# Kernel tuning notes

Measured on AMD Instinct MI355X. Metric: run time of the kernel, lower is better.

Reference implementation:

```python
import jax, jax.numpy as jnp
import numpy as np
from math import factorial

# ---- static sizes from S2ConvNet_original ----
B_IN, B1, B2 = 30, 10, 6   # bandwidths: input S2 grid, after conv1 (SO3), after conv2 (SO3)
F1, F2, FOUT = 20, 40, 10
BATCH = 128


def _wigner_d(l, beta):
    """Wigner small-d matrix d^l_{m',m}(beta); rows m'=-l..l, cols m=-l..l."""
    cb, sb = np.cos(beta / 2.0), np.sin(beta / 2.0)
    d = np.zeros((2 * l + 1, 2 * l + 1))
    for i, mp in enumerate(range(-l, l + 1)):
        for j, m in enumerate(range(-l, l + 1)):
            pref = np.sqrt(float(factorial(l + mp) * factorial(l - mp) * factorial(l + m) * factorial(l - m)))
            acc = 0.0
            for s in range(max(0, m - mp), min(l + m, l - mp) + 1):
                den = factorial(l + m - s) * factorial(s) * factorial(mp - m + s) * factorial(l - mp - s)
                acc += ((-1.0) ** (mp - m + s) / den) * cb ** (2 * l + m - mp - 2 * s) * sb ** (mp - m + 2 * s)
            d[i, j] = pref * acc
    return d


def _dh_quad(b):
    """Driscoll-Healy beta grid / weights: sum_j w_j g(beta_j) ~ int_0^pi g(b) sin(b) db."""
    j = np.arange(2 * b)
    beta = np.pi * (2 * j + 1) / (4 * b)
    k = np.arange(b)[:, None]
    w = (2.0 / b) * np.sin(beta) * np.sum(np.sin((2 * k + 1) * beta[None, :]) / (2 * k + 1), axis=0)
    return beta, w


def _s2_grid(max_beta=np.pi / 8, n_alpha=8, n_beta=3):
    beta = np.arange(1, n_beta + 1) * max_beta / n_beta
    alpha = np.linspace(0, 2 * np.pi, n_alpha, endpoint=False)
    Bm, Am = np.meshgrid(beta, alpha, indexing='ij')
    return np.stack([Bm.ravel(), Am.ravel()], 1)  # [24, 2]


def _so3_grid(max_beta=np.pi / 8, max_gamma=2 * np.pi, n_alpha=8, n_beta=3, n_gamma=8):
    beta = np.arange(1, n_beta + 1) * max_beta / n_beta
    alpha = np.linspace(0, 2 * np.pi, n_alpha, endpoint=False)
    pre_gamma = np.linspace(0, max_gamma, n_gamma, endpoint=False)
    Bm, Am, Cm = np.meshgrid(beta, alpha, pre_gamma, indexing='ij')
    return np.stack([Bm.ravel(), Am.ravel(), (Cm - Am).ravel()], 1)  # [192, 3]


# ---------- conv1: S2 analysis (b 30 -> 10) ----------
_beta30, _qw30 = _dh_quad(B_IN)
_A1 = np.concatenate(
    [np.stack([_wigner_d(l, bb)[:, l] for bb in _beta30])  # d^l_{m,0}(beta_j): [60, 2l+1]
     * (_qw30 * (2 * np.pi / (2 * B_IN)))[:, None]
     for l in range(B1)], axis=1)  # [60, 100]
_A1J = jnp.asarray(_A1.astype(np.float32))
_M1 = np.concatenate([np.arange(-l, l + 1) for l in range(B1)])
_M1_IDX = np.mod(_M1, 2 * B_IN)

_g1 = _s2_grid()
_Y1 = np.concatenate(
    [np.stack([_wigner_d(l, bb)[:, l] for bb in _g1[:, 0]])
     * np.exp(-1j * np.outer(_g1[:, 1], np.arange(-l, l + 1)))
     for l in range(B1)], axis=1)  # [24, 100] complex
_Y1J = jnp.asarray(_Y1.astype(np.complex64))
_SC1 = float(1.0 / np.sqrt(len(_g1) * 1 * (B1 ** 4) / (B_IN ** 2)))

# ---------- SO3 synthesis tables at b=10 ----------
_beta10, _qw10 = _dh_quad(B1)
_D1S = [jnp.asarray(((2 * l + 1) * np.stack([_wigner_d(l, bb) for bb in _beta10])).astype(np.float32)) for l in range(B1)]
_FM1 = [np.mod(np.arange(-l, l + 1), 2 * B1) for l in range(B1)]

# ---------- conv2: SO3 analysis (b 10 -> 6) ----------
_W3 = np.concatenate(
    [(np.stack([_wigner_d(l, bb) for bb in _beta10])  # [20, 2l+1, 2l+1]
      * (_qw10 * (2 * np.pi / (2 * B1)) ** 2)[:, None, None]).reshape(2 * B1, -1)
     for l in range(B2)], axis=1)  # [20, 286]
_W3J = jnp.asarray(_W3.astype(np.float32))
_M2 = np.concatenate([np.repeat(np.arange(-l, l + 1), 2 * l + 1) for l in range(B2)])
_N2 = np.concatenate([np.tile(np.arange(-l, l + 1), 2 * l + 1) for l in range(B2)])
_M2_IDX = np.mod(_M2, 2 * B1)
_N2_IDX = np.mod(_N2, 2 * B1)

_g2 = _so3_grid()
_Y2 = np.concatenate(
    [np.stack([_wigner_d(l, bb) for bb in _g2[:, 0]]).reshape(len(_g2), -1)
     * (np.exp(-1j * np.outer(_g2[:, 1], np.arange(-l, l + 1)))[:, :, None]
        * np.exp(-1j * np.outer(_g2[:, 2], np.arange(-l, l + 1)))[:, None, :]).reshape(len(_g2), -1)
     for l in range(B2)], axis=1)  # [192, 286] complex: D^l_{mn}(alpha,beta,gamma)
_Y2J = jnp.asarray(_Y2.astype(np.complex64))
_SC2 = float(1.0 / np.sqrt(len(_g2) * F1 * (B2 ** 3) / (B1 ** 3)))

# ---------- SO3 synthesis tables at b=6 + integration weights ----------
_beta6, _qw6 = _dh_quad(B2)
_D2S = [jnp.asarray(((2 * l + 1) * np.stack([_wigner_d(l, bb) for bb in _beta6])).astype(np.float32)) for l in range(B2)]
_FM2 = [np.mod(np.arange(-l, l + 1), 2 * B2) for l in range(B2)]
_W_INT = jnp.asarray((_qw6 * (2 * np.pi / (2 * B2)) ** 2).astype(np.float32))


def _forward(x, k1, bias1, k2, bias2, w_out, b_lin):
    Bn = x.shape[0]
    # ===== conv1: S2 correlation -> function on SO(3) at b=10 =====
    xf = jnp.fft.fft(x.astype(jnp.complex64), axis=-1)                 # FFT over alpha: [B,1,60,60]
    xhat = jnp.einsum('bfjs,js->sbf', xf[..., _M1_IDX], _A1J)          # [100,B,1] S2 spectrum
    k1h = jnp.einsum('iop,ps->sio', (k1 * _SC1).astype(jnp.complex64), _Y1J)  # [100,1,F1]
    Ffreq = jnp.zeros((Bn, F1, 2 * B1, 2 * B1, 2 * B1), jnp.complex64)  # [B,F1,beta,m,n]
    for l in range(B1):
        s0, s1 = l * l, (l + 1) * (l + 1)
        # z^l_{mn} = sum_fin xhat^l_m conj(khat^l_n)  (outer product per degree l)
        zl = jnp.einsum('mbi,nio->bmno', xhat[s0:s1], jnp.conj(k1h[s0:s1]))
        fb = jnp.einsum('bmno,jmn->bojmn', zl, _D1S[l])                # (2l+1) d^l_{mn}(beta_j)
        Ffreq = Ffreq.at[:, :, :, _FM1[l][:, None], _FM1[l][None, :]].add(fb)
    x1 = jnp.fft.ifft2(Ffreq, axes=(-2, -1)).real * float((2 * B1) ** 2)  # synth over alpha,gamma
    x1 = jax.nn.relu(x1 + bias1[None, :, None, None, None])            # [B,F1,20,20,20]
    # ===== conv2: SO(3) correlation -> b=6 =====
    x1f = jnp.fft.fft2(x1.astype(jnp.complex64), axes=(-2, -1))        # FFT over alpha,gamma
    xhat2 = jnp.einsum('bfjs,js->sbf', x1f[:, :, :, _M2_IDX, _N2_IDX], _W3J)  # [286,B,F1]
    k2h = jnp.einsum('iop,ps->sio', (k2 * _SC2).astype(jnp.complex64), _Y2J)  # [286,F1,F2]
    Ffreq2 = jnp.zeros((Bn, F2, 2 * B2, 2 * B2, 2 * B2), jnp.complex64)
    base = 0
    for l in range(B2):
        L = 2 * l + 1
        xl = xhat2[base:base + L * L].reshape(L, L, Bn, F1)            # [m,k,B,Fin]
        gl = jnp.conj(k2h[base:base + L * L].reshape(L, L, F1, F2))    # [n,k,Fin,Fout]
        zl = jnp.einsum('mkbi,nkio->bmno', xl, gl)                     # z^l = xhat^l ghat^l^H
        fb = jnp.einsum('bmno,jmn->bojmn', zl, _D2S[l])
        Ffreq2 = Ffreq2.at[:, :, :, _FM2[l][:, None], _FM2[l][None, :]].add(fb)
        base += L * L
    x2 = jnp.fft.ifft2(Ffreq2, axes=(-2, -1)).real * float((2 * B2) ** 2)
    x2 = jax.nn.relu(x2 + bias2[None, :, None, None, None])            # [B,F2,12,12,12]
    # ===== so3_integrate + linear head =====
    feat = jnp.einsum('bfjkp,j->bf', x2, _W_INT)                       # [B,F2]
    return feat @ w_out.T + b_lin


def setup_inputs() -> dict:
    key = jax.random.key(0)
    ks = jax.random.split(key, 4)
    return {
        'x': jax.random.normal(ks[0], (BATCH, 1, 2 * B_IN, 2 * B_IN), jnp.float32),
        'k1': jax.random.normal(ks[1], (1, F1, len(_g1)), jnp.float32),
        'bias1': jnp.zeros((F1,), jnp.float32),
        'k2': jax.random.normal(ks[2], (F1, F2, len(_g2)), jnp.float32),
        'bias2': jnp.zeros((F2,), jnp.float32),
        'w_out': jax.random.normal(ks[3], (FOUT, F2), jnp.float32) / np.sqrt(F2).astype(np.float32),
        'b_lin': jnp.zeros((FOUT,), jnp.float32),
    }


def reference(x, k1, bias1, k2, bias2, w_out, b_lin):
    return _forward(x, k1, bias1, k2, bias2, w_out, b_lin)
```

## Files before the change

kernel.cpp:

```cpp
#include <hip/hip_runtime.h>
#include <math.h>

#define PI_D 3.14159265358979323846

#define BATCH 128
#define F1 20
#define F2 40
#define FOUT 10
#define NS1 100
#define NS2 286
#define NH2 146

typedef float v2f __attribute__((ext_vector_type(2)));
#define PKFMA(a,b,c) __builtin_elementwise_fma((a),(b),(c))
#define SW(v) __builtin_shufflevector((v),(v),1,0)
static __device__ __forceinline__ v2f bc2(float s){ return (v2f){s,s}; }
static __device__ __forceinline__ v2f ldv(const float2* p){ return *(const v2f*)p; }

#define GLOAD_LDS16(g,l) __builtin_amdgcn_global_load_lds( \
  (const __attribute__((address_space(1))) void*)(g), \
  (__attribute__((address_space(3))) void*)(l), 16, 0, 0)

__constant__ int ZB10c[11] = {0,1,10,35,84,165,286,455,680,969,1330};
__constant__ int B2OFFc[7] = {0,1,10,35,84,165,286};
__constant__ int HOFFc[7]  = {0,1,6,19,44,85,146};
__constant__ float2 E8c[8] = {
  { 1.f, 0.f}, { 0.70710678118654752f,-0.70710678118654752f},
  { 0.f,-1.f}, {-0.70710678118654752f,-0.70710678118654752f},
  {-1.f, 0.f}, {-0.70710678118654752f, 0.70710678118654752f},
  { 0.f, 1.f}, { 0.70710678118654752f, 0.70710678118654752f}};

#define WFENCE do{ __builtin_amdgcn_sched_barrier(0); \
  asm volatile("s_waitcnt lgkmcnt(0)" ::: "memory"); \
  __builtin_amdgcn_sched_barrier(0); }while(0)

__device__ inline void h_decode(int h, int& l, int& m, int& n){
  l=0; while(HOFFc[l+1]<=h) ++l;
  int r=h-HOFFc[l], L=2*l+1;
  if(r<l+1){ n=0; m=r; }
  else { int q=r-(l+1); n=q/L+1; m=q%L-l; }
}

__device__ inline double ipow_d(double x, int n){ double r=1.0; for(int i=0;i<n;++i) r*=x; return r; }
__device__ inline double dfact(int n){ double r=1.0; for(int i=2;i<=n;++i) r*=(double)i; return r; }

__device__ double wigd(int l, int mp, int m, double beta){
  double cb=cos(0.5*beta), sb=sin(0.5*beta);
  double pref=sqrt(dfact(l+mp)*dfact(l-mp)*dfact(l+m)*dfact(l-m));
  int s0 = (m-mp>0) ? (m-mp) : 0;
  int s1 = (l+m < l-mp) ? (l+m) : (l-mp);
  double acc=0.0;
  for(int s=s0;s<=s1;++s){
    double den=dfact(l+m-s)*dfact(s)*dfact(mp-m+s)*dfact(l-mp-s);
    double t=ipow_d(cb,2*l+m-mp-2*s)*ipow_d(sb,mp-m+2*s)/den;
    acc += ((mp-m+s)&1)? -t : t;
  }
  return pref*acc;
}

__device__ double dhw(int b, int j){
  double beta=PI_D*(2*j+1)/(4.0*b);
  double s=0.0;
  for(int k=0;k<b;++k) s += sin((2*k+1)*beta)/(2*k+1);
  return (2.0/b)*sin(beta)*s;
}

__device__ inline float2 cmulc(float2 a, float2 b){
  return make_float2(a.x*b.x + a.y*b.y, a.y*b.x - a.x*b.y);
}

__global__ void gen_all(float* A1, float* D1SJ, float* W3H, float* D2SJ,
                        float* D3_2, float* D3_1, float* WINT,
                        float2* E60, float2* E20, float2* E12,
                        unsigned* zLUT, unsigned* xh2LUT, unsigned* h2LUT,
                        unsigned short* fhLUT, unsigned* aLUT){
  __shared__ double dhwS[60];
  int blk=blockIdx.x, t=threadIdx.x;
  if(blk<24){
    if(t<60) dhwS[t]=dhw(30,t);
    __syncthreads();
    int idx=blk*256+t;
    if(idx<6000){
      int j=idx/NS1, s=idx%NS1;
      int l=0; while((l+1)*(l+1)<=s) ++l;
      int m=s-l*l-l;
      double beta=PI_D*(2*j+1)/120.0;
      A1[idx]=(float)(wigd(l,m,0,beta)*dhwS[j]*(2.0*PI_D/60.0));
    }
  } else if(blk<76){
    int idx=(blk-24)*256+t; if(idx>=13300) return;
    int j=idx/1330, s=idx%1330;
    int l=0; while(ZB10c[l+1]<=s) ++l;
    int r=s-ZB10c[l]; int L=2*l+1;
    int mi=r/L, ni=r%L;
    double beta=PI_D*(2*j+1)/40.0;
    float v=(float)((2*l+1)*wigd(l,mi-l,ni-l,beta));
    D1SJ[j*1330+s]=v;
    int s2=ZB10c[l]+(2*l-mi)*L+ni;
    D1SJ[(19-j)*1330+s2]=(ni&1)? -v : v;
  } else if(blk<82){
    if(t<20) dhwS[t]=dhw(10,t);
    __syncthreads();
    int idx=(blk-76)*256+t;
    if(idx<10*NH2){
      int j=idx/NH2, h=idx%NH2;
      int l,m,n; h_decode(h,l,m,n);
      double beta=PI_D*(2*j+1)/40.0;
      double c=2.0*PI_D/20.0;
      float v=(float)(wigd(l,m,n,beta)*dhwS[j]*c*c);
      W3H[j*NH2+h]=v;
      if(n==0){
        W3H[(19-j)*NH2+h]=((l+m)&1)? -v : v;
      } else {
        int L=2*l+1;
        int hp=HOFFc[l]+(l+1)+(n-1)*L+(l-m);
        W3H[(19-j)*NH2+hp]=((l+n)&1)? -v : v;
      }
    }
  } else if(blk<89){
    int idx=(blk-82)*256+t; if(idx>=1716) return;
    int j=idx/286, s=idx%286;
    int l=0; while(B2OFFc[l+1]<=s) ++l;
    int r=s-B2OFFc[l]; int L=2*l+1;
    int mi=r/L, ni=r%L;
    double beta=PI_D*(2*j+1)/24.0;
    float v=(float)((2*l+1)*wigd(l,mi-l,ni-l,beta));
    D2SJ[j*286+s]=v;
    int s2=B2OFFc[l]+(2*l-mi)*L+ni;
    D2SJ[(11-j)*286+s2]=(ni&1)? -v : v;
  } else if(blk<93){
    int idx=(blk-89)*256+t; if(idx>=3*286) return;
    int bi=idx/286, s=idx%286;
    int l=0; while(B2OFFc[l+1]<=s) ++l;
    int r=s-B2OFFc[l]; int L=2*l+1;
    int mi=r/L, ni=r%L;
    double beta=(bi+1)*(PI_D/8.0)/3.0;
    D3_2[idx]=(float)wigd(l,mi-l,ni-l,beta);
  } else if(blk<95){
    int idx=(blk-93)*256+t; if(idx>=3*100) return;
    int bi=idx/100, s=idx%100;
    int l=0; while((l+1)*(l+1)<=s) ++l;
    int m=s-l*l-l;
    double beta=(bi+1)*(PI_D/8.0)/3.0;
    D3_1[idx]=(float)wigd(l,m,0,beta);
  } else if(blk==95){
    if(t<12){ double c=2.0*PI_D/12.0; WINT[t]=(float)(dhw(6,t)*c*c); }
    if(t<60){ double a=2.0*PI_D*t/60.0; E60[t]=make_float2((float)cos(a),(float)sin(a)); }
    if(t<20){ double a=2.0*PI_D*t/20.0; E20[t]=make_float2((float)cos(a),(float)sin(a)); }
    if(t<12){ double a=2.0*PI_D*t/12.0; E12[t]=make_float2((float)cos(a),(float)sin(a)); }
  } else if(blk<102){
    int idx=(blk-96)*256+t; if(idx>=1330) return;
    int l=0; while(ZB10c[l+1]<=idx) ++l;
    int r=idx-ZB10c[l], L=2*l+1;
    int mi=r/L, ni=r%L;
    unsigned s1x=(unsigned)(l*l+mi), s1k=(unsigned)(l*l+ni);
    zLUT[idx]=s1x|(s1k<<16);
  } else if(blk==102){
    if(t<146){
      int l,m,n; h_decode(t,l,m,n);
      int L=2*l+1;
      int s2 =B2OFFc[l]+(m+l)*L+(n+l);
      int s2p=B2OFFc[l]+(l-m)*L+(l-n);
      unsigned sg=(unsigned)((m+n)&1);
      xh2LUT[t]=(unsigned)s2 | ((unsigned)s2p<<10) | (sg<<20);
      h2LUT[t]=(unsigned)l | ((unsigned)(m+l)<<4) | ((unsigned)(n+l)<<8) | ((unsigned)s2<<12);
      fhLUT[t]=(unsigned short)((n==0)? m : 6+(n-1)*11+(m+5));
    }
  } else {
    if(t==0){
      int idx=0;
      for(int lm=0;lm<10;++lm){
        for(int m=0;m<10;++m){
          int nlo=(m==0)?0:-9;
          for(int n=nlo;n<10;++n){
            int an=n<0?-n:n;
            int lmin=m>an?m:an;
            if(lmin!=lm) continue;
            int L=2*lm+1;
            int zi=ZB10c[lm]+(m+lm)*L+(n+lm);
            aLUT[idx++]=(unsigned)zi | ((unsigned)m<<11) | ((unsigned)(n+9)<<15) | ((unsigned)lm<<20);
          }
        }
      }
    }
  }
}

__global__ __launch_bounds__(256) void front_k(const float* __restrict__ x,
    const float* __restrict__ k1, const float* __restrict__ k2,
    const float2* __restrict__ E60, const float* __restrict__ A1,
    const float* __restrict__ D3_1,
    float2* __restrict__ XHAT, float2* __restrict__ K1H, float2* __restrict__ KA){
  __shared__ float2 E8s[8];
  int blk=blockIdx.x, t=threadIdx.x;
  if(blk<128){
    __shared__ __align__(16) float xs[3600];
    __shared__ float2 E60s[60];
    __shared__ float2 XFs[1140];
    if(t<60){ float2 e=E60[t]; E60s[t]=make_float2(e.x,-e.y); }
    {
      const float4* src=(const float4*)(x+blk*3600);
      float4* dst=(float4*)xs;
      for(int i=t;i<900;i+=256) GLOAD_LDS16(src+i, dst+(i&~63));
    }
    __syncthreads();
    for(int idx=t; idx<1140; idx+=256){
      int j=idx/19, mi=idx%19;
      int step=(mi<9)? mi+51 : mi-9;
      bool modd = ((mi&1)==0);
      const float* xr=xs+j*60;
      v2f acc={0.f,0.f};
      int k=0;
      for(int a=0;a<30;++a){
        float xv = modd ? (xr[a]-xr[a+30]) : (xr[a]+xr[a+30]);
        acc=PKFMA(bc2(xv), ldv(&E60s[k]), acc);
        k+=step; if(k>=60)k-=60;
      }
      XFs[idx]=make_float2(acc.x,acc.y);
    }
    __syncthreads();
    for(int s=t; s<100; s+=256){
      int l=0; while((l+1)*(l+1)<=s) ++l;
      int m=s-l*l-l;
      const float2* xf=&XFs[m+9];
      v2f acc={0.f,0.f};
      for(int j=0;j<60;++j){
        acc=PKFMA(bc2(A1[j*NS1+s]), ldv(&xf[j*19]), acc);
      }
      XHAT[blk*NS1+s]=make_float2(acc.x,acc.y);
    }
  } else if(blk<136){
    if(t<8) E8s[t]=E8c[t];
    __syncthreads();
    int idx=(blk-128)*256+t;
    if(idx<F1*NS1){
      int o=idx/NS1, s=idx%NS1;
      int l=0; while((l+1)*(l+1)<=s) ++l;
      int m=s-l*l-l;
      int mm=m&7;
      v2f acc={0.f,0.f};
      for(int bi=0;bi<3;++bi){
        v2f sum={0.f,0.f};
        int q=0;
        #pragma unroll
        for(int ai=0;ai<8;++ai){
          sum=PKFMA(bc2(k1[o*24+bi*8+ai]), ldv(&E8s[q]), sum);
          q=(q+mm)&7;
        }
        acc=PKFMA(bc2(D3_1[bi*100+s]), sum, acc);
      }
      const float SC1f = 0.06123724356957945f;
      K1H[idx]=make_float2(acc.x*SC1f, acc.y*SC1f);
    }
  } else {
    if(t<8) E8s[t]=E8c[t];
    __syncthreads();
    int idx=(blk-136)*256+t;
    if(idx<153600){
      int ai=idx&7, q=(idx>>3)&7;
      int r2=idx>>6;
      int bi=r2%3, io=r2/3;
      const float* kp=k2+(size_t)io*192+bi*64+ai*8;
      v2f acc={0.f,0.f};
      int ph=0;
      #pragma unroll
      for(int gi=0;gi<8;++gi){
        acc=PKFMA(bc2(kp[gi]), ldv(&E8s[ph]), acc);
        ph=(ph+q)&7;
      }
      KA[(size_t)io*192+bi*64+q*8+ai]=make_float2(acc.x,acc.y);
    }
  }
}

__global__ __launch_bounds__(512,6) void fused1(
    const float2* __restrict__ XHAT, const float2* __restrict__ K1H,
    const float* __restrict__ D1SJ, const float* __restrict__ W3H,
    const float2* __restrict__ E20, const float* __restrict__ bias1,
    const unsigned* __restrict__ zLUT, const unsigned* __restrict__ xh2LUT,
    const unsigned short* __restrict__ fhLUT, const unsigned* __restrict__ aLUT,
    float2* __restrict__ XH2){
  const int b=blockIdx.x, o=blockIdx.y, t=threadIdx.x;
  const int ln=t&63, w=t>>6;
  __shared__ __align__(16) float2 zS[1330];
  __shared__ __align__(16) float2 TWE2[400];
  __shared__ __align__(16) float2 regA[8][200];
  __shared__ __align__(16) float2 regB[8][190];

  for(int idx=t; idx<400; idx+=512){
    int r=idx/20, c=idx%20;
    TWE2[idx]=E20[(r*c)%20];
  }
  {
    float2* st=regA[0];
    if(t<100) st[t]=XHAT[b*NS1+t];
    else if(t<200) st[t]=K1H[o*NS1+(t-100)];
  }
  __syncthreads();
  {
    const float2* st=regA[0];
    for(int idx=t; idx<1330; idx+=512){
      unsigned u=zLUT[idx];
      v2f xa=ldv(&st[u&0xffff]);
      v2f kb=ldv(&st[100+(u>>16)]);
      v2f p1=xa*kb, p2=xa*SW(kb);
      zS[idx]=make_float2(p1.x+p1.y, p2.y-p2.x);
    }
  }
  __syncthreads();

  const float bb1=bias1[o];
  float2* G  = regA[w];
  float*  vbF= (float*)regA[w];
  float2* Fq = regA[w];
  float*  RB = (float*)regB[w];
  float*  Sx = RB;
  float*  Sy = RB+180;
  float*  T0f= RB+360;
  float2* U_T= regB[w];
  v2f fa0={0.f,0.f}, fa1=fa0, fa2=fa0;

  const int BROW[19]={11,12,13,14,15,16,17,18,19,0,1,2,3,4,5,6,7,8,9};

  for(int jq=0;jq<3;++jq){
    const int j=jq*8+w;
    const bool act=(j<20);
    const float* Dg=D1SJ + (act? j*1330 : 0);
    if(act) for(int idx=ln; idx<181; idx+=64){
      unsigned au=aLUT[idx];
      int zi=au&2047;
      int m=(au>>11)&15, n9=(au>>15)&31, l=(au>>20)&15;
      int L=2*l+1;
      int m2=2*m+2;
      v2f a0={0.f,0.f};
      for(; l<10; ++l){
        a0=PKFMA(ldv(&zS[zi]), bc2(Dg[zi]), a0);
        zi += L*L + 2*L + m2; L += 2;
      }
      *(v2f*)&G[m*19+n9]=a0;
    }
    WFENCE;
    if(act){
    if(ln<45){
      int mb=ln/5+1, gp=(ln%5)*2;
      const float2* Gr=&G[mb*19];
      v2f E1a={0.f,0.f},E2a=E1a,O1a=E1a,O2a=E1a;
      v2f E1b=E1a,E2b=E1a,O1b=E1a,O2b=E1a;
      #pragma unroll
      for(int c=0;c<19;++c){
        v2f gv=ldv(&Gr[c]);
        const float* er=(const float*)&TWE2[BROW[c]*20+gp];
        float4 e01=*(const float4*)er;
        v2f e0={e01.x,e01.y}, e1={e01.z,e01.w};
        if(c&1){
          E1a=PKFMA(gv,e0,E1a); E2a=PKFMA(gv,SW(e0),E2a);
          E1b=PKFMA(gv,e1,E1b); E2b=PKFMA(gv,SW(e1),E2b);
        } else {
          O1a=PKFMA(gv,e0,O1a); O2a=PKFMA(gv,SW(e0),O2a);
          O1b=PKFMA(gv,e1,O1b); O2b=PKFMA(gv,SW(e1),O2b);
        }
      }
      int si=(mb-1)*20+gp;
      float exa=E1a.x-E1a.y, oxa=O1a.x-O1a.y;
      float eya=E2a.x+E2a.y, oya=O2a.x+O2a.y;
      float exb=E1b.x-E1b.y, oxb=O1b.x-O1b.y;
      float eyb=E2b.x+E2b.y, oyb=O2b.x+O2b.y;
      *(v2f*)&Sx[si]   =(v2f){2.f*(exa+oxa), 2.f*(exb+oxb)};
      *(v2f*)&Sx[si+10]=(v2f){2.f*(exa-oxa), 2.f*(exb-oxb)};
      *(v2f*)&Sy[si]   =(v2f){2.f*(eya+oya), 2.f*(eyb+oyb)};
      *(v2f*)&Sy[si+10]=(v2f){2.f*(eya-oya), 2.f*(eyb-oyb)};
    } else if(ln<50){
      int gt=(ln-45)*2;
      float g0x=G[9].x;
      float Ea=0.f,Eb=0.f,Oa=0.f,Ob=0.f;
      #pragma unroll
      for(int n=1;n<10;++n){
        float2 gv=G[9+n];
        const float* er=(const float*)&TWE2[n*20+gt];
        float4 e01=*(const float4*)er;
        float ra=gv.x*e01.x-gv.y*e01.y;
        float rb=gv.x*e01.z-gv.y*e01.w;
        if((n&1)==0){ Ea+=ra; Eb+=rb; } else { Oa+=ra; Ob+=rb; }
      }
      T0f[gt]   =g0x+2.f*(Ea+Oa);
      T0f[gt+1] =g0x+2.f*(Eb+Ob);
      T0f[gt+10]=g0x+2.f*(Ea-Oa);
      T0f[gt+11]=g0x+2.f*(Eb-Ob);
    }
    }
    WFENCE;
    if(act && ln<50){
      int a=ln/5, g0=(ln%5)*4;
      v2f i01={T0f[g0]+bb1, T0f[g0+1]+bb1};
      v2f i23={T0f[g0+2]+bb1, T0f[g0+3]+bb1};
      v2f P01={0.f,0.f},P23=P01,Q01=P01,Q23=P01;
      #pragma unroll
      for(int m=1;m<10;++m){
        float2 e=TWE2[a*20+m];
        v2f sx01=*(const v2f*)&Sx[(m-1)*20+g0];
        v2f sx23=*(const v2f*)&Sx[(m-1)*20+g0+2];
        v2f sy01=*(const v2f*)&Sy[(m-1)*20+g0];
        v2f sy23=*(const v2f*)&Sy[(m-1)*20+g0+2];
        if(m&1){
          Q01=PKFMA(bc2(e.x),sx01,Q01); Q01=PKFMA(bc2(-e.y),sy01,Q01);
          Q23=PKFMA(bc2(e.x),sx23,Q23); Q23=PKFMA(bc2(-e.y),sy23,Q23);
        } else {
          P01=PKFMA(bc2(e.x),sx01,P01); P01=PKFMA(bc2(-e.y),sy01,P01);
          P23=PKFMA(bc2(e.x),sx23,P23); P23=PKFMA(bc2(-e.y),sy23,P23);
        }
      }
      v2f z2={0.f,0.f};
      v2f vA01=i01+P01+Q01, vA23=i23+P23+Q23;
      v2f vB01=i01+P01-Q01, vB23=i23+P23-Q23;
      *(v2f*)&vbF[a*20+g0]       =__builtin_elementwise_max(vA01,z2);
      *(v2f*)&vbF[a*20+g0+2]     =__builtin_elementwise_max(vA23,z2);
      *(v2f*)&vbF[(a+10)*20+g0]  =__builtin_elementwise_max(vB01,z2);
      *(v2f*)&vbF[(a+10)*20+g0+2]=__builtin_elementwise_max(vB23,z2);
    }
    WFENCE;
    if(act && ln<60){
      int a=ln/3, np=ln%3;
      int nu0=2*np, nu1=2*np+1;
      int r0=(np==0)?0:(20-2*np);
      int r1=19-2*np;
      const float* vp=&vbF[a*20];
      const float2* T0r=&TWE2[r0*20];
      const float2* T1r=&TWE2[r1*20];
      v2f u0={0.f,0.f}, u1=u0;
      #pragma unroll
      for(int g=0;g<10;++g){
        float va=vp[g], vb=vp[g+10];
        u0=PKFMA(bc2(va+vb), ldv(&T0r[g]), u0);
        u1=PKFMA(bc2(va-vb), ldv(&T1r[g]), u1);
      }
      *(v2f*)&U_T[nu0*20+a]=u0; *(v2f*)&U_T[nu1*20+a]=u1;
    }
    WFENCE;
    if(act && ln<61){
      int mu,nu;
      if(ln<6){ mu=ln; nu=0; } else { int q=ln-6; nu=q/11+1; mu=q%11-5; }
      int mm=(mu+20)%20;
      int rm=(20-mm)%20;
      bool modd=(mm&1);
      const float2* Ur=&U_T[nu*20];
      const float2* Er=&TWE2[rm*20];
      v2f p1={0.f,0.f}, p2=p1;
      #pragma unroll
      for(int a=0;a<10;++a){
        v2f ua=ldv(&Ur[a]), ub=ldv(&Ur[a+10]);
        v2f u = modd ? (ua-ub) : (ua+ub);
        v2f e=ldv(&Er[a]);
        p1=PKFMA(u,e,p1);
        p2=PKFMA(u,SW(e),p2);
      }
      Fq[ln]=make_float2(p1.x-p1.y, p2.x+p2.y);
    }
    WFENCE;
    if(act){
      const float* W3r=W3H + j*NH2;
      fa0=PKFMA(bc2(W3r[ln]),    ldv(&Fq[fhLUT[ln]]),    fa0);
      fa1=PKFMA(bc2(W3r[64+ln]), ldv(&Fq[fhLUT[64+ln]]), fa1);
      if(ln<18) fa2=PKFMA(bc2(W3r[128+ln]), ldv(&Fq[fhLUT[128+ln]]), fa2);
    }
    WFENCE;
  }
  regB[w][ln]=make_float2(fa0.x,fa0.y);
  regB[w][64+ln]=make_float2(fa1.x,fa1.y);
  if(ln<18) regB[w][128+ln]=make_float2(fa2.x,fa2.y);
  __syncthreads();
  for(int h=t; h<146; h+=512){
    unsigned u=xh2LUT[h];
    int s2=u&1023, s2p=(u>>10)&1023;
    float sg=((u>>20)&1)? -1.f : 1.f;
    float2 a0=regB[0][h], a1=regB[1][h], a2=regB[2][h], a3=regB[3][h];
    float2 a4=regB[4][h], a5=regB[5][h], a6=regB[6][h], a7=regB[7][h];
    float2 a=make_float2(a0.x+a1.x+a2.x+a3.x+a4.x+a5.x+a6.x+a7.x,
                         a0.y+a1.y+a2.y+a3.y+a4.y+a5.y+a6.y+a7.y);
    XH2[(b*286+s2 )*F1+o]=a;
    XH2[(b*286+s2p)*F1+o]=make_float2(sg*a.x, -sg*a.y);
  }
}

__global__ __launch_bounds__(192) void k2h_k(const float2* __restrict__ KA,
                      const float* __restrict__ D3_2,
                      const unsigned* __restrict__ h2LUT, const unsigned* __restrict__ xh2LUT,
                      float2* __restrict__ K2H){
  __shared__ float2 kaS[192];
  __shared__ float2 E8s[8];
  int io=blockIdx.x, t=threadIdx.x;
  int i=io/F2, o=io%F2;
  if(t<8) E8s[t]=E8c[t];
  kaS[t]=KA[(size_t)io*192+t];
  __syncthreads();
  if(t>=146) return;
  unsigned hu=h2LUT[t];
  int l=hu&15, mi=(hu>>4)&15, ni=(hu>>8)&15, s2=hu>>12;
  int m=mi-l, n=ni-l;
  unsigned xu=xh2LUT[t];
  int s2p=(xu>>10)&1023;
  float sg=((xu>>20)&1)? -1.f : 1.f;
  int q=n&7, p=(m-n)&7;
  v2f a1={0.f,0.f}, a2=a1;
  for(int bi=0;bi<3;++bi){
    const float2* kp=&kaS[bi*64+q*8];
    v2f s1={0.f,0.f}, s2v=s1;
    int ph=0;
    #pragma unroll
    for(int ai=0;ai<8;++ai){
      v2f ka=ldv(&kp[ai]), e=ldv(&E8s[ph]);
      s1=PKFMA(ka,e,s1); s2v=PKFMA(ka,SW(e),s2v);
      ph=(ph+p)&7;
    }
    v2f dv=bc2(D3_2[bi*286+s2]);
    a1=PKFMA(dv,s1,a1); a2=PKFMA(dv,s2v,a2);
  }
  const float SC2f = 0.034722222222222224f;
  float re=(a1.x-a1.y)*SC2f, im=(a2.x+a2.y)*SC2f;
  K2H[((size_t)o*286+s2)*F1+i]=make_float2(re,im);
  K2H[((size_t)o*286+s2p)*F1+i]=make_float2(sg*re,-sg*im);
}

__global__ __launch_bounds__(256,3) void fused2(
    const float2* __restrict__ XH2, const float2* __restrict__ K2H,
    const float* __restrict__ D2SJ, const float* __restrict__ WINT,
    const float2* __restrict__ E12, const float* __restrict__ bias2,
    const unsigned* __restrict__ h2LUT, const unsigned* __restrict__ xh2LUT,
    float* __restrict__ FEAT){
  const int b=blockIdx.x, o=blockIdx.y, t=threadIdx.x;
  const int ln=t&63, w=t>>6;
  __shared__ __align__(16) float2 Xs[2420];
  __shared__ __align__(16) float2 Ks[2420];
  __shared__ float2 zpS[1144];
  __shared__ float2 z2S[286];
  __shared__ float  redS[256];
  float2* alias=(float2*)Xs;
  float2* TWE12=alias;

  const int gb[4]={0,84,165,286};
  const int hb[4]={0,44,85,146};
  for(int grp=0; grp<3; ++grp){
    int row0=gb[grp], rows=gb[grp+1]-row0;
    {
      int cnt4=rows*10;
      const float4* xsrc=(const float4*)(XH2+(size_t)(b*286+row0)*F1);
      const float4* ksrc=(const float4*)(K2H+(size_t)(o*286+row0)*F1);
      float4* xd=(float4*)Xs; float4* kd=(float4*)Ks;
      for(int i4=t;i4<cnt4;i4+=256){
        int wb=i4&~63;
        GLOAD_LDS16(xsrc+i4, xd+wb);
        GLOAD_LDS16(ksrc+i4, kd+wb);
      }
    }
    __syncthreads();
    int nh=hb[grp+1]-hb[grp];
    for(int idx=t; idx<4*nh; idx+=256){
      int hl=idx>>2, iq=idx&3;
      int h=hb[grp]+hl;
      unsigned hu=h2LUT[h];
      int l=hu&15, mi=(hu>>4)&15, ni=(hu>>8)&15, s2=hu>>12;
      int L=2*l+1;
      int xr0=(B2OFFc[l]-row0)+mi*L;
      int kr0=(B2OFFc[l]-row0)+ni*L;
      v2f p1={0.f,0.f}, p2=p1;
      for(int k=0;k<L;++k){
        const float2* xp=Xs+(xr0+k)*F1+iq*5;
        const float2* kp=Ks+(kr0+k)*F1+iq*5;
        #pragma unroll
        for(int i=0;i<5;++i){
          v2f xa=ldv(&xp[i]), kb=ldv(&kp[i]);
          p1=PKFMA(xa,kb,p1);
          p2=PKFMA(xa,SW(kb),p2);
        }
      }
      zpS[iq*286+s2]=make_float2(p1.x+p1.y, p2.y-p2.x);
    }
    __syncthreads();
  }
  for(int idx=t; idx<146; idx+=256){
    unsigned xu=xh2LUT[idx];
    int s2=xu&1023, s2p=(xu>>10)&1023;
    float sg=((xu>>20)&1)? -1.f : 1.f;
    float2 a;
    a.x=zpS[0*286+s2].x+zpS[1*286+s2].x+zpS[2*286+s2].x+zpS[3*286+s2].x;
    a.y=zpS[0*286+s2].y+zpS[1*286+s2].y+zpS[2*286+s2].y+zpS[3*286+s2].y;
    z2S[s2]=a;
    z2S[s2p]=make_float2(sg*a.x,-sg*a.y);
  }
  __syncthreads();
  for(int idx=t; idx<144; idx+=256){
    int r=idx/12, c=idx%12;
    TWE12[idx]=E12[(r*c)%12];
  }
  __syncthreads();

  float2* base2=alias+144+w*400;
  float2* G2_0=base2; float2* G2_1=base2+66; float2* G2_2=base2+132;
  float*  SP=(float*)(base2+198);
  float*  S2x0=SP, *S2x1=SP+60, *S2x2=SP+120;
  float*  S2y0=SP+180, *S2y1=SP+240, *S2y2=SP+300;
  float*  T02=SP+360;
  float personal=0.f;
  const float b2v=bias2[o];
  const int j0=3*w, j1=3*w+1, j2=3*w+2;
  const float* Dg0=D2SJ + j0*286;
  const float* Dg1=D2SJ + j1*286;
  const float* Dg2=D2SJ + j2*286;
  const int BR12[11]={7,8,9,10,11,0,1,2,3,4,5};

  if(ln<61){
    int m,n;
    if(ln<6){m=0;n=ln;} else {int qq=ln-6;m=qq/11+1;n=qq%11-5;}
    int an=n<0?-n:n; int l=m>an?m:an; int L=2*l+1;
    int zi=B2OFFc[l]+(m+l)*L+(n+l); int m2=2*m+2;
    v2f a0={0.f,0.f}, a1=a0, a2=a0;
    for(;l<6;++l){
      v2f zv=ldv(&z2S[zi]);
      a0=PKFMA(zv, bc2(Dg0[zi]), a0);
      a1=PKFMA(zv, bc2(Dg1[zi]), a1);
      a2=PKFMA(zv, bc2(Dg2[zi]), a2);
      zi+=L*L+2*L+m2; L+=2;
    }
    int gi=m*11+(n+5);
    *(v2f*)&G2_0[gi]=a0; *(v2f*)&G2_1[gi]=a1; *(v2f*)&G2_2[gi]=a2;
  }
  WFENCE;
  if(ln<30){
    int m=ln/6+1, g=(ln%6)*2;
    v2f p10={0.f,0.f},p20=p10,p11=p10,p21=p10;
    v2f q10=p10,q20=p10,q11=p10,q21=p10;
    v2f r10=p10,r20=p10,r11=p10,r21=p10;
    #pragma unroll
    for(int c=0;c<11;++c){
      float4 eq=*(const float4*)&TWE12[BR12[c]*12+g];
      v2f e0={eq.x,eq.y}, e1={eq.z,eq.w};
      v2f g0=ldv(&G2_0[m*11+c]), g1=ldv(&G2_1[m*11+c]), g2=ldv(&G2_2[m*11+c]);
      p10=PKFMA(g0,e0,p10); p20=PKFMA(g0,SW(e0),p20);
      p11=PKFMA(g0,e1,p11); p21=PKFMA(g0,SW(e1),p21);
      q10=PKFMA(g1,e0,q10); q20=PKFMA(g1,SW(e0),q20);
      q11=PKFMA(g1,e1,q11); q21=PKFMA(g1,SW(e1),q21);
      r10=PKFMA(g2,e0,r10); r20=PKFMA(g2,SW(e0),r20);
      r11=PKFMA(g2,e1,r11); r21=PKFMA(g2,SW(e1),r21);
    }
    int si=(m-1)*12+g;
    S2x0[si]=2.f*(p10.x-p10.y); S2x0[si+1]=2.f*(p11.x-p11.y);
    S2y0[si]=2.f*(p20.x+p20.y); S2y0[si+1]=2.f*(p21.x+p21.y);
    S2x1[si]=2.f*(q10.x-q10.y); S2x1[si+1]=2.f*(q11.x-q11.y);
    S2y1[si]=2.f*(q20.x+q20.y); S2y1[si+1]=2.f*(q21.x+q21.y);
    S2x2[si]=2.f*(r10.x-r10.y); S2x2[si+1]=2.f*(r11.x-r11.y);
    S2y2[si]=2.f*(r20.x+r20.y); S2y2[si+1]=2.f*(r21.x+r21.y);
  } else if(ln<42){
    int g=ln-30;
    float r0=G2_0[5].x, r1=G2_1[5].x, r2=G2_2[5].x;
    #pragma unroll
    for(int n=1;n<6;++n){
      float2 e=TWE12[n*12+g];
      float2 g0=G2_0[5+n], g1=G2_1[5+n], g2=G2_2[5+n];
      r0+=2.f*(g0.x*e.x-g0.y*e.y);
      r1+=2.f*(g1.x*e.x-g1.y*e.y);
      r2+=2.f*(g2.x*e.x-g2.y*e.y);
    }
    T02[g]=r0; T02[12+g]=r1; T02[24+g]=r2;
  }
  WFENCE;
  if(ln<36){
    float w0=WINT[j0], w1=WINT[j1], w2=WINT[j2];
    int a=ln/3, g4=(ln%3)*4;
    v2f iA0={T02[g4]+b2v, T02[g4+1]+b2v},       iB0={T02[g4+2]+b2v, T02[g4+3]+b2v};
    v2f iA1={T02[12+g4]+b2v, T02[12+g4+1]+b2v}, iB1={T02[12+g4+2]+b2v, T02[12+g4+3]+b2v};
    v2f iA2={T02[24+g4]+b2v, T02[24+g4+1]+b2v}, iB2={T02[24+g4+2]+b2v, T02[24+g4+3]+b2v};
    #pragma unroll
    for(int m=1;m<6;++m){
      float2 e=TWE12[a*12+m];
      v2f ex=bc2(e.x), eny=bc2(-e.y);
      int si=(m-1)*12+g4;
      v2f sx, sy;
      sx=*(const v2f*)&S2x0[si];   sy=*(const v2f*)&S2y0[si];
      iA0=PKFMA(ex,sx,iA0); iA0=PKFMA(eny,sy,iA0);
      sx=*(const v2f*)&S2x0[si+2]; sy=*(const v2f*)&S2y0[si+2];
      iB0=PKFMA(ex,sx,iB0); iB0=PKFMA(eny,sy,iB0);
      sx=*(const v2f*)&S2x1[si];   sy=*(const v2f*)&S2y1[si];
      iA1=PKFMA(ex,sx,iA1); iA1=PKFMA(eny,sy,iA1);
      sx=*(const v2f*)&S2x1[si+2]; sy=*(const v2f*)&S2y1[si+2];
      iB1=PKFMA(ex,sx,iB1); iB1=PKFMA(eny,sy,iB1);
      sx=*(const v2f*)&S2x2[si];   sy=*(const v2f*)&S2y2[si];
      iA2=PKFMA(ex,sx,iA2); iA2=PKFMA(eny,sy,iA2);
      sx=*(const v2f*)&S2x2[si+2]; sy=*(const v2f*)&S2y2[si+2];
      iB2=PKFMA(ex,sx,iB2); iB2=PKFMA(eny,sy,iB2);
    }
    v2f z2={0.f,0.f};
    v2f rA0=__builtin_elementwise_max(iA0,z2), rB0=__builtin_elementwise_max(iB0,z2);
    v2f rA1=__builtin_elementwise_max(iA1,z2), rB1=__builtin_elementwise_max(iB1,z2);
    v2f rA2=__builtin_elementwise_max(iA2,z2), rB2=__builtin_elementwise_max(iB2,z2);
    personal += w0*(rA0.x+rA0.y+rB0.x+rB0.y)
              + w1*(rA1.x+rA1.y+rB1.x+rB1.y)
              + w2*(rA2.x+rA2.y+rB2.x+rB2.y);
  }
  redS[t]=personal;
  __syncthreads();
  for(int s=128;s>0;s>>=1){
    if(t<s) redS[t]+=redS[t+s];
    __syncthreads();
  }
  if(t==0) FEAT[b*F2+o]=redS[0];
}

__global__ void head_k(const float* __restrict__ FEAT, const float* __restrict__ w_out,
                       const float* __restrict__ b_lin, float* __restrict__ out){
  int idx=blockIdx.x*blockDim.x+threadIdx.x;
  if(idx>=BATCH*FOUT) return;
  int b=idx/FOUT, q=idx%FOUT;
  float acc=b_lin[q];
  for(int f=0;f<F2;++f) acc += FEAT[b*F2+f]*w_out[q*F2+f];
  out[idx]=acc;
}

extern "C" void kernel_launch(void* const* d_in, const int* in_sizes, int n_in,
                              void* d_out, int out_size, void* d_ws, size_t ws_size,
                              hipStream_t stream) {
  const float* x    =(const float*)d_in[0];
  const float* k1   =(const float*)d_in[1];
  const float* bias1=(const float*)d_in[2];
  const float* k2   =(const float*)d_in[3];
  const float* bias2=(const float*)d_in[4];
  const float* w_out=(const float*)d_in[5];
  const float* b_lin=(const float*)d_in[6];
  float* out=(float*)d_out;

  char* ws=(char*)d_ws;
  float*  A1   =(float* )(ws+0);
  float*  D1SJ =(float* )(ws+24000);
  float*  W3H  =(float* )(ws+130400);
  float*  D2SJ =(float* )(ws+142080);
  float*  D3_2 =(float* )(ws+155808);
  float*  D3_1 =(float* )(ws+159248);
  float*  WINT =(float* )(ws+160448);
  float2* E60  =(float2*)(ws+160496);
  float2* E20  =(float2*)(ws+160976);
  float2* E12  =(float2*)(ws+161136);
  unsigned* zLUT=(unsigned*)(ws+161248);
  unsigned* xh2LUT=(unsigned*)(ws+166576);
  unsigned* h2LUT =(unsigned*)(ws+167160);
  unsigned short* fhLUT=(unsigned short*)(ws+167744);
  unsigned* aLUT =(unsigned*)(ws+168048);
  float2* XHAT =(float2*)(ws+168784);
  float2* K1H  =(float2*)(ws+271184);
  float2* KA   =(float2*)(ws+287184);
  float2* XH2  =(float2*)(ws+1515984);
  float2* K2H  =(float2*)(ws+7373264);
  float*  FEAT =(float* )(ws+9203664);

  (void)in_sizes; (void)n_in; (void)out_size; (void)ws_size;

  gen_all<<<104,256,0,stream>>>(A1,D1SJ,W3H,D2SJ,D3_2,D3_1,WINT,E60,E20,E12,
                                zLUT,xh2LUT,h2LUT,fhLUT,aLUT);
  front_k<<<736,256,0,stream>>>(x,k1,k2,E60,A1,D3_1,XHAT,K1H,KA);
  dim3 g1(BATCH,F1);
  fused1<<<g1,512,0,stream>>>(XHAT,K1H,D1SJ,W3H,E20,bias1,zLUT,xh2LUT,fhLUT,aLUT,XH2);
  k2h_k<<<F1*F2,192,0,stream>>>(KA,D3_2,h2LUT,xh2LUT,K2H);
  dim3 g2(BATCH,F2);
  fused2<<<g2,256,0,stream>>>(XH2,K2H,D2SJ,WINT,E12,bias2,h2LUT,xh2LUT,FEAT);
  head_k<<<(BATCH*FOUT+255)/256,256,0,stream>>>(FEAT,w_out,b_lin,out);
}
```

Baseline: 212.8 us.

## Tabulate factorials, move k2 transform to gen_all, transpose XH2/K2H layout, split DFT

Replaces repeated factorial loops in the Wigner-d generator with a shared-memory factorial table. Moves the k2 angular DFT from front_k into gen_all so it runs alongside table generation. Changes the XH2 and K2H layout from frequency-major to channel-major so their writes are contiguous per row. fused2 then loads them with a strided scalar gather into padded 21-wide LDS rows instead of async 16-byte global-to-LDS loads. It also rewrites the 12-point gamma DFT in fused2 as an even/odd split that halves the twiddle loads, at the risk of a slower, less coalesced fused2 load phase.

Measured after the change: 237.2 us. 11.5% more time.

```diff
diff --git a/kernel.cpp b/kernel.cpp
--- a/kernel.cpp
+++ b/kernel.cpp
@@ -42,16 +42,15 @@
 }
 
 __device__ inline double ipow_d(double x, int n){ double r=1.0; for(int i=0;i<n;++i) r*=x; return r; }
-__device__ inline double dfact(int n){ double r=1.0; for(int i=2;i<=n;++i) r*=(double)i; return r; }
-
-__device__ double wigd(int l, int mp, int m, double beta){
+
+__device__ double wigd_t(int l, int mp, int m, double beta, const double* F){
   double cb=cos(0.5*beta), sb=sin(0.5*beta);
-  double pref=sqrt(dfact(l+mp)*dfact(l-mp)*dfact(l+m)*dfact(l-m));
+  double pref=sqrt(F[l+mp]*F[l-mp]*F[l+m]*F[l-m]);
   int s0 = (m-mp>0) ? (m-mp) : 0;
   int s1 = (l+m < l-mp) ? (l+m) : (l-mp);
   double acc=0.0;
   for(int s=s0;s<=s1;++s){
-    double den=dfact(l+m-s)*dfact(s)*dfact(mp-m+s)*dfact(l-mp-s);
+    double den=F[l+m-s]*F[s]*F[mp-m+s]*F[l-mp-s];
     double t=ipow_d(cb,2*l+m-mp-2*s)*ipow_d(sb,mp-m+2*s)/den;
     acc += ((mp-m+s)&1)? -t : t;
   }
@@ -65,27 +64,31 @@
   return (2.0/b)*sin(beta)*s;
 }
 
-__device__ inline float2 cmulc(float2 a, float2 b){
-  return make_float2(a.x*b.x + a.y*b.y, a.y*b.x - a.x*b.y);
-}
-
-__global__ void gen_all(float* A1, float* D1SJ, float* W3H, float* D2SJ,
+__global__ void gen_all(const float* __restrict__ k2,
+                        float* A1, float* D1SJ, float* W3H, float* D2SJ,
                         float* D3_2, float* D3_1, float* WINT,
                         float2* E60, float2* E20, float2* E12,
                         unsigned* zLUT, unsigned* xh2LUT, unsigned* h2LUT,
-                        unsigned short* fhLUT, unsigned* aLUT){
+                        unsigned short* fhLUT, unsigned* aLUT,
+                        float2* KA){
+  __shared__ double factS[21];
   __shared__ double dhwS[60];
+  __shared__ float2 E8L[8];
   int blk=blockIdx.x, t=threadIdx.x;
+  if(t==0){ double f=1.0; factS[0]=1.0; for(int k=1;k<=20;++k){ f*=(double)k; factS[k]=f; } }
+  if(blk<24){ if(t<60) dhwS[t]=dhw(30,t); }
+  else if(blk>=76 && blk<82){ if(t<20) dhwS[t]=dhw(10,t); }
+  if(t<8) E8L[t]=E8c[t];
+  __syncthreads();
+  const double* F=factS;
   if(blk<24){
-    if(t<60) dhwS[t]=dhw(30,t);
-    __syncthreads();
     int idx=blk*256+t;
     if(idx<6000){
       int j=idx/NS1, s=idx%NS1;
       int l=0; while((l+1)*(l+1)<=s) ++l;
       int m=s-l*l-l;
       double beta=PI_D*(2*j+1)/120.0;
-      A1[idx]=(float)(wigd(l,m,0,beta)*dhwS[j]*(2.0*PI_D/60.0));
+      A1[idx]=(float)(wigd_t(l,m,0,beta,F)*dhwS[j]*(2.0*PI_D/60.0));
     }
   } else if(blk<76){
     int idx=(blk-24)*256+t; if(idx>=13300) return;
@@ -94,20 +97,18 @@
     int r=s-ZB10c[l]; int L=2*l+1;
     int mi=r/L, ni=r%L;
     double beta=PI_D*(2*j+1)/40.0;
-    float v=(float)((2*l+1)*wigd(l,mi-l,ni-l,beta));
+    float v=(float)((2*l+1)*wigd_t(l,mi-l,ni-l,beta,F));
     D1SJ[j*1330+s]=v;
     int s2=ZB10c[l]+(2*l-mi)*L+ni;
     D1SJ[(19-j)*1330+s2]=(ni&1)? -v : v;
   } else if(blk<82){
-    if(t<20) dhwS[t]=dhw(10,t);
-    __syncthreads();
     int idx=(blk-76)*256+t;
     if(idx<10*NH2){
       int j=idx/NH2, h=idx%NH2;
       int l,m,n; h_decode(h,l,m,n);
       double beta=PI_D*(2*j+1)/40.0;
       double c=2.0*PI_D/20.0;
-      float v=(float)(wigd(l,m,n,beta)*dhwS[j]*c*c);
+      float v=(float)(wigd_t(l,m,n,beta,F)*dhwS[j]*c*c);
       W3H[j*NH2+h]=v;
       if(n==0){
         W3H[(19-j)*NH2+h]=((l+m)&1)? -v : v;
@@ -124,7 +125,7 @@
     int r=s-B2OFFc[l]; int L=2*l+1;
     int mi=r/L, ni=r%L;
     double beta=PI_D*(2*j+1)/24.0;
-    float v=(float)((2*l+1)*wigd(l,mi-l,ni-l,beta));
+    float v=(float)((2*l+1)*wigd_t(l,mi-l,ni-l,beta,F));
     D2SJ[j*286+s]=v;
     int s2=B2OFFc[l]+(2*l-mi)*L+ni;
     D2SJ[(11-j)*286+s2]=(ni&1)? -v : v;
@@ -135,14 +136,14 @@
     int r=s-B2OFFc[l]; int L=2*l+1;
     int mi=r/L, ni=r%L;
     double beta=(bi+1)*(PI_D/8.0)/3.0;
-    D3_2[idx]=(float)wigd(l,mi-l,ni-l,beta);
+    D3_2[idx]=(float)wigd_t(l,mi-l,ni-l,beta,F);
   } else if(blk<95){
     int idx=(blk-93)*256+t; if(idx>=3*100) return;
     int bi=idx/100, s=idx%100;
     int l=0; while((l+1)*(l+1)<=s) ++l;
     int m=s-l*l-l;
     double beta=(bi+1)*(PI_D/8.0)/3.0;
-    D3_1[idx]=(float)wigd(l,m,0,beta);
+    D3_1[idx]=(float)wigd_t(l,m,0,beta,F);
   } else if(blk==95){
     if(t<12){ double c=2.0*PI_D/12.0; WINT[t]=(float)(dhw(6,t)*c*c); }
     if(t<60){ double a=2.0*PI_D*t/60.0; E60[t]=make_float2((float)cos(a),(float)sin(a)); }
@@ -166,7 +167,7 @@
       h2LUT[t]=(unsigned)l | ((unsigned)(m+l)<<4) | ((unsigned)(n+l)<<8) | ((unsigned)s2<<12);
       fhLUT[t]=(unsigned short)((n==0)? m : 6+(n-1)*11+(m+5));
     }
-  } else {
+  } else if(blk==103){
     if(t==0){
       int idx=0;
       for(int lm=0;lm<10;++lm){
@@ -183,15 +184,30 @@
         }
       }
     }
+  } else {
+    int idx=(blk-104)*256+t;
+    if(idx<153600){
+      int ai=idx&7, q=(idx>>3)&7;
+      int r2=idx>>6;
+      int bi=r2%3, io=r2/3;
+      const float* kp=k2+(size_t)io*192+bi*64+ai*8;
+      v2f acc={0.f,0.f};
+      int ph=0;
+      #pragma unroll
+      for(int gi=0;gi<8;++gi){
+        acc=PKFMA(bc2(kp[gi]), ldv(&E8L[ph]), acc);
+        ph=(ph+q)&7;
+      }
+      KA[(size_t)io*192+bi*64+q*8+ai]=make_float2(acc.x,acc.y);
+    }
   }
 }
 
 __global__ __launch_bounds__(256) void front_k(const float* __restrict__ x,
-    const float* __restrict__ k1, const float* __restrict__ k2,
+    const float* __restrict__ k1,
     const float2* __restrict__ E60, const float* __restrict__ A1,
     const float* __restrict__ D3_1,
-    float2* __restrict__ XHAT, float2* __restrict__ K1H, float2* __restrict__ KA){
-  __shared__ float2 E8s[8];
+    float2* __restrict__ XHAT, float2* __restrict__ K1H){
   int blk=blockIdx.x, t=threadIdx.x;
   if(blk<128){
     __shared__ __align__(16) float xs[3600];
@@ -229,7 +245,8 @@
       }
       XHAT[blk*NS1+s]=make_float2(acc.x,acc.y);
     }
-  } else if(blk<136){
+  } else {
+    __shared__ float2 E8s[8];
     if(t<8) E8s[t]=E8c[t];
     __syncthreads();
     int idx=(blk-128)*256+t;
@@ -251,24 +268,6 @@
       }
       const float SC1f = 0.06123724356957945f;
       K1H[idx]=make_float2(acc.x*SC1f, acc.y*SC1f);
-    }
-  } else {
-    if(t<8) E8s[t]=E8c[t];
-    __syncthreads();
-    int idx=(blk-136)*256+t;
-    if(idx<153600){
-      int ai=idx&7, q=(idx>>3)&7;
-      int r2=idx>>6;
-      int bi=r2%3, io=r2/3;
-      const float* kp=k2+(size_t)io*192+bi*64+ai*8;
-      v2f acc={0.f,0.f};
-      int ph=0;
-      #pragma unroll
-      for(int gi=0;gi<8;++gi){
-        acc=PKFMA(bc2(kp[gi]), ldv(&E8s[ph]), acc);
-        ph=(ph+q)&7;
-      }
-      KA[(size_t)io*192+bi*64+q*8+ai]=make_float2(acc.x,acc.y);
     }
   }
 }
@@ -468,6 +467,7 @@
   regB[w][64+ln]=make_float2(fa1.x,fa1.y);
   if(ln<18) regB[w][128+ln]=make_float2(fa2.x,fa2.y);
   __syncthreads();
+  float2* XHrow=XH2+(size_t)(b*F1+o)*286;
   for(int h=t; h<146; h+=512){
     unsigned u=xh2LUT[h];
     int s2=u&1023, s2p=(u>>10)&1023;
@@ -476,8 +476,8 @@
     float2 a4=regB[4][h], a5=regB[5][h], a6=regB[6][h], a7=regB[7][h];
     float2 a=make_float2(a0.x+a1.x+a2.x+a3.x+a4.x+a5.x+a6.x+a7.x,
                          a0.y+a1.y+a2.y+a3.y+a4.y+a5.y+a6.y+a7.y);
-    XH2[(b*286+s2 )*F1+o]=a;
-    XH2[(b*286+s2p)*F1+o]=make_float2(sg*a.x, -sg*a.y);
+    XHrow[s2 ]=a;
+    XHrow[s2p]=make_float2(sg*a.x, -sg*a.y);
   }
 }
 
@@ -516,8 +516,9 @@
   }
   const float SC2f = 0.034722222222222224f;
   float re=(a1.x-a1.y)*SC2f, im=(a2.x+a2.y)*SC2f;
-  K2H[((size_t)o*286+s2)*F1+i]=make_float2(re,im);
-  K2H[((size_t)o*286+s2p)*F1+i]=make_float2(sg*re,-sg*im);
+  float2* Krow=K2H+(size_t)(o*F1+i)*286;
+  Krow[s2 ]=make_float2(re,im);
+  Krow[s2p]=make_float2(sg*re,-sg*im);
 }
 
 __global__ __launch_bounds__(256,3) void fused2(
@@ -528,8 +529,8 @@
     float* __restrict__ FEAT){
   const int b=blockIdx.x, o=blockIdx.y, t=threadIdx.x;
   const int ln=t&63, w=t>>6;
-  __shared__ __align__(16) float2 Xs[2420];
-  __shared__ __align__(16) float2 Ks[2420];
+  __shared__ __align__(16) float2 Xs[2541];
+  __shared__ __align__(16) float2 Ks[2541];
   __shared__ float2 zpS[1144];
   __shared__ float2 z2S[286];
   __shared__ float  redS[256];
@@ -541,14 +542,13 @@
   for(int grp=0; grp<3; ++grp){
     int row0=gb[grp], rows=gb[grp+1]-row0;
     {
-      int cnt4=rows*10;
-      const float4* xsrc=(const float4*)(XH2+(size_t)(b*286+row0)*F1);
-      const float4* ksrc=(const float4*)(K2H+(size_t)(o*286+row0)*F1);
-      float4* xd=(float4*)Xs; float4* kd=(float4*)Ks;
-      for(int i4=t;i4<cnt4;i4+=256){
-        int wb=i4&~63;
-        GLOAD_LDS16(xsrc+i4, xd+wb);
-        GLOAD_LDS16(ksrc+i4, kd+wb);
+      int cnt=20*rows;
+      const float2* xbase=XH2+(size_t)b*F1*286+row0;
+      const float2* kbase=K2H+(size_t)o*F1*286+row0;
+      for(int idx=t; idx<cnt; idx+=256){
+        int i=idx/rows, sl=idx-i*rows;
+        Xs[sl*21+i]=xbase[i*286+sl];
+        Ks[sl*21+i]=kbase[i*286+sl];
       }
     }
     __syncthreads();
@@ -563,8 +563,8 @@
       int kr0=(B2OFFc[l]-row0)+ni*L;
       v2f p1={0.f,0.f}, p2=p1;
       for(int k=0;k<L;++k){
-        const float2* xp=Xs+(xr0+k)*F1+iq*5;
-        const float2* kp=Ks+(kr0+k)*F1+iq*5;
+        const float2* xp=Xs+(xr0+k)*21+iq*5;
+        const float2* kp=Ks+(kr0+k)*21+iq*5;
         #pragma unroll
         for(int i=0;i<5;++i){
           v2f xa=ldv(&xp[i]), kb=ldv(&kp[i]);
@@ -625,29 +625,44 @@
   }
   WFENCE;
   if(ln<30){
-    int m=ln/6+1, g=(ln%6)*2;
-    v2f p10={0.f,0.f},p20=p10,p11=p10,p21=p10;
-    v2f q10=p10,q20=p10,q11=p10,q21=p10;
-    v2f r10=p10,r20=p10,r11=p10,r21=p10;
+    int m=ln/6+1, g=ln%6;
+    v2f E1_0={0.f,0.f},E2_0=E1_0,O1_0=E1_0,O2_0=E1_0;
+    v2f E1_1=E1_0,E2_1=E1_0,O1_1=E1_0,O2_1=E1_0;
+    v2f E1_2=E1_0,E2_2=E1_0,O1_2=E1_0,O2_2=E1_0;
     #pragma unroll
     for(int c=0;c<11;++c){
-      float4 eq=*(const float4*)&TWE12[BR12[c]*12+g];
-      v2f e0={eq.x,eq.y}, e1={eq.z,eq.w};
+      float2 ef=TWE12[BR12[c]*12+g];
+      v2f e={ef.x,ef.y};
       v2f g0=ldv(&G2_0[m*11+c]), g1=ldv(&G2_1[m*11+c]), g2=ldv(&G2_2[m*11+c]);
-      p10=PKFMA(g0,e0,p10); p20=PKFMA(g0,SW(e0),p20);
-      p11=PKFMA(g0,e1,p11); p21=PKFMA(g0,SW(e1),p21);
-      q10=PKFMA(g1,e0,q10); q20=PKFMA(g1,SW(e0),q20);
-      q11=PKFMA(g1,e1,q11); q21=PKFMA(g1,SW(e1),q21);
-      r10=PKFMA(g2,e0,r10); r20=PKFMA(g2,SW(e0),r20);
-      r11=PKFMA(g2,e1,r11); r21=PKFMA(g2,SW(e1),r21);
+      if(c&1){
+        E1_0=PKFMA(g0,e,E1_0); E2_0=PKFMA(g0,SW(e),E2_0);
+        E1_1=PKFMA(g1,e,E1_1); E2_1=PKFMA(g1,SW(e),E2_1);
+        E1_2=PKFMA(g2,e,E1_2); E2_2=PKFMA(g2,SW(e),E2_2);
+      } else {
+        O1_0=PKFMA(g0,e,O1_0); O2_0=PKFMA(g0,SW(e),O2_0);
+        O1_1=PKFMA(g1,e,O1_1); O2_1=PKFMA(g1,SW(e),O2_1);
+        O1_2=PKFMA(g2,e,O1_2); O2_2=PKFMA(g2,SW(e),O2_2);
+      }
     }
     int si=(m-1)*12+g;
-    S2x0[si]=2.f*(p10.x-p10.y); S2x0[si+1]=2.f*(p11.x-p11.y);
-    S2y0[si]=2.f*(p20.x+p20.y); S2y0[si+1]=2.f*(p21.x+p21.y);
-    S2x1[si]=2.f*(q10.x-q10.y); S2x1[si+1]=2.f*(q11.x-q11.y);
-    S2y1[si]=2.f*(q20.x+q20.y); S2y1[si+1]=2.f*(q21.x+q21.y);
-    S2x2[si]=2.f*(r10.x-r10.y); S2x2[si+1]=2.f*(r11.x-r11.y);
-    S2y2[si]=2.f*(r20.x+r20.y); S2y2[si+1]=2.f*(r21.x+r21.y);
+    {
+      float Ex=E1_0.x-E1_0.y, Ox=O1_0.x-O1_0.y;
+      float Ey=E2_0.x+E2_0.y, Oy=O2_0.x+O2_0.y;
+      S2x0[si]=2.f*(Ex+Ox); S2x0[si+6]=2.f*(Ex-Ox);
+      S2y0[si]=2.f*(Ey+Oy); S2y0[si+6]=2.f*(Ey-Oy);
+    }
+    {
+      float Ex=E1_1.x-E1_1.y, Ox=O1_1.x-O1_1.y;
+      float Ey=E2_1.x+E2_1.y, Oy=O2_1.x+O2_1.y;
+      S2x1[si]=2.f*(Ex+Ox); S2x1[si+6]=2.f*(Ex-Ox);
+      S2y1[si]=2.f*(Ey+Oy); S2y1[si+6]=2.f*(Ey-Oy);
+    }
+    {
+      float Ex=E1_2.x-E1_2.y, Ox=O1_2.x-O1_2.y;
+      float Ey=E2_2.x+E2_2.y, Oy=O2_2.x+O2_2.y;
+      S2x2[si]=2.f*(Ex+Ox); S2x2[si+6]=2.f*(Ex-Ox);
+      S2y2[si]=2.f*(Ey+Oy); S2y2[si+6]=2.f*(Ey-Oy);
+    }
   } else if(ln<42){
     int g=ln-30;
     float r0=G2_0[5].x, r1=G2_1[5].x, r2=G2_2[5].x;
@@ -751,9 +766,9 @@
 
   (void)in_sizes; (void)n_in; (void)out_size; (void)ws_size;
 
-  gen_all<<<104,256,0,stream>>>(A1,D1SJ,W3H,D2SJ,D3_2,D3_1,WINT,E60,E20,E12,
-                                zLUT,xh2LUT,h2LUT,fhLUT,aLUT);
-  front_k<<<736,256,0,stream>>>(x,k1,k2,E60,A1,D3_1,XHAT,K1H,KA);
+  gen_all<<<704,256,0,stream>>>(k2,A1,D1SJ,W3H,D2SJ,D3_2,D3_1,WINT,E60,E20,E12,
+                                zLUT,xh2LUT,h2LUT,fhLUT,aLUT,KA);
+  front_k<<<136,256,0,stream>>>(x,k1,E60,A1,D3_1,XHAT,K1H);
   dim3 g1(BATCH,F1);
   fused1<<<g1,512,0,stream>>>(XHAT,K1H,D1SJ,W3H,E20,bias1,zLUT,xh2LUT,fhLUT,aLUT,XH2);
   k2h_k<<<F1*F2,192,0,stream>>>(KA,D3_2,h2LUT,xh2LUT,K2H);
```
